# Performance work log

Hardware: AMD Instinct MI355X
Metric: run time of the kernel (lower is better)

Reference implementation:

```python
import jax, jax.numpy as jnp
import numpy as np


def setup_inputs() -> dict:
    key = jax.random.key(0)
    ks = jax.random.split(key, 6)
    B, Nu, Ni, D = 256, 512, 512, 64
    u_fea = jax.random.normal(ks[0], (B, Nu, D), dtype=jnp.float32)
    i_fea = jax.random.normal(ks[1], (B, Ni, D), dtype=jnp.float32)
    M = jax.random.normal(ks[2], (D, D), dtype=jnp.float32)
    # Linear weights, torch-style: y = x @ W.T + b (init scaled like torch default)
    lim = 1.0 / np.sqrt(D)
    Wu = jax.random.uniform(ks[3], (D, D), minval=-lim, maxval=lim, dtype=jnp.float32)
    Wi = jax.random.uniform(ks[4], (D, D), minval=-lim, maxval=lim, dtype=jnp.float32)
    bu = jnp.zeros((D,), dtype=jnp.float32)
    bi = jnp.zeros((D,), dtype=jnp.float32)
    return {"u_fea": u_fea, "i_fea": i_fea, "M": M, "Wu": Wu, "bu": bu, "Wi": Wi, "bi": bi}


def reference(u_fea, i_fea, M, Wu, bu, Wi, bi):
    # fc_u / fc_i: torch Linear is x @ W.T + b
    u = jnp.einsum('bud,ed->bue', u_fea, Wu) + bu   # [B, Nu, D]
    i = jnp.einsum('bid,ed->bie', i_fea, Wi) + bi   # [B, Ni, D]
    # Bilinear co-attention score S = u @ M @ i^T  -> [B, Nu, Ni]
    uM = jnp.einsum('bud,de->bue', u, M)
    S = jnp.einsum('bue,bie->bui', uM, i)
    # pooling == 'max'
    u_score = S.max(axis=2)   # [B, Nu]
    i_score = S.max(axis=1)   # [B, Ni]
    # gumbel == False -> plain softmax over the review axis
    p_u = jax.nn.softmax(u_score, axis=1)
    p_i = jax.nn.softmax(i_score, axis=1)
    return (p_u[:, :, None], p_i[:, :, None])
```

## Files before the change

kernel.cpp:

```cpp
#include <hip/hip_runtime.h>
#include <float.h>


#define NBATCH 256
#define NSEQ   512
#define DIM    64

typedef __attribute__((ext_vector_type(8))) short short8;
typedef __attribute__((ext_vector_type(4))) float f32x4;

#define MFMA16(a,b,c) __builtin_amdgcn_mfma_f32_16x16x32_bf16(a,b,c,0,0,0)

__device__ __forceinline__ void cvt2(float f, unsigned short &h, unsigned short &l) {
    unsigned u = __float_as_uint(f);
    unsigned hb = (u + 0x7FFFu + ((u >> 16) & 1u)) >> 16;
    h = (unsigned short)hb;
    float r = f - __uint_as_float(hb << 16);
    unsigned u2 = __float_as_uint(r);
    l = (unsigned short)((u2 + 0x7FFFu + ((u2 >> 16) & 1u)) >> 16);
}

__device__ __forceinline__ void cvt8(const f32x4 a, const f32x4 b, short8 &hi, short8 &lo) {
    unsigned short h, l;
    #pragma unroll
    for (int i = 0; i < 4; ++i) { cvt2(a[i], h, l); hi[i] = (short)h; lo[i] = (short)l; }
    #pragma unroll
    for (int i = 0; i < 4; ++i) { cvt2(b[i], h, l); hi[4+i] = (short)h; lo[4+i] = (short)l; }
}

__global__ __launch_bounds__(64) void coatt_prep1(
    const float* __restrict__ M, const float* __restrict__ Wi,
    const float* __restrict__ bi, float* __restrict__ ws)
{
    __shared__ float Ml[64];
    const int d = blockIdx.x, f = threadIdx.x;
    Ml[f] = M[d*64 + f];
    __syncthreads();
    float s = 0.f;
    #pragma unroll 8
    for (int e = 0; e < 64; ++e) s = fmaf(Ml[e], Wi[e*64 + f], s);
    ws[8448 + d*64 + f] = s;
    float p = Ml[f] * bi[f];
    #pragma unroll
    for (int off = 1; off < 64; off <<= 1) p += __shfl_xor(p, off, 64);
    if (f == 0) ws[12544 + d] = p;
}

__global__ __launch_bounds__(64) void coatt_prep2(
    const float* __restrict__ Wu, const float* __restrict__ bu,
    float* __restrict__ ws)
{
    __shared__ float col[64];
    const int c = blockIdx.x, f = threadIdx.x;
    const float* T = ws + 8448;
    col[f] = Wu[f*64 + c];
    __syncthreads();
    float s = 0.f;
    #pragma unroll 8
    for (int d = 0; d < 64; ++d) s = fmaf(col[d], T[d*64 + f], s);
    unsigned short* efh = (unsigned short*)(ws + 4352);
    unsigned short* efl = efh + 4096;
    unsigned short h, l;
    cvt2(s, h, l);
    const int ko = c >> 5, quad = (c >> 3) & 3, j = c & 7;
    const int ft = f >> 4, f15 = f & 15;
    const int p = ft*1024 + ko*512 + (quad*16 + f15)*8 + j;
    efh[p] = h; efl[p] = l;
    float pa = col[f] * ws[12544 + f];
    #pragma unroll
    for (int off = 1; off < 64; off <<= 1) pa += __shfl_xor(pa, off, 64);
    if (f == 0) ws[4096 + c] = pa;
    if (c == 0) {
        float sg = 0.f;
        #pragma unroll 8
        for (int d = 0; d < 64; ++d) sg = fmaf(bu[d], T[d*64 + f], sg);
        ws[4160 + f] = sg;
        float ps = bu[f] * ws[12544 + f];
        #pragma unroll
        for (int off = 1; off < 64; off <<= 1) ps += __shfl_xor(ps, off, 64);
        if (f == 0) ws[4224] = ps;
    }
}

#define LDS_BYTES 151552

__global__ __launch_bounds__(512, 2) void coatt_main(
    const float* __restrict__ u_fea, const float* __restrict__ i_fea,
    const float* __restrict__ ws, float* __restrict__ out)
{
    extern __shared__ char sm[];
    unsigned short* YH = (unsigned short*)sm;
    unsigned short* YL = (unsigned short*)(sm + 65536);
    const int t    = threadIdx.x;
    const int lane = t & 63, w = t >> 6, quad = lane >> 4, l15 = lane & 15;
    float* Xsw    = (float*)(sm + 131072) + w * 576;
    float* rl     = (float*)(sm + 149504);
    float* colp   = (float*)(sm + 131072);
    float* uscore = (float*)(sm + 147456);
    float* red    = (float*)(sm + 149504);

    const int b = blockIdx.x;
    const float* ub = u_fea + (size_t)b * NSEQ * DIM;
    const float* ib = i_fea + (size_t)b * NSEQ * DIM;

    const unsigned short* efh = (const unsigned short*)(ws + 4352);
    const unsigned short* efl = efh + 4096;
    short8 EH[4][2], EL[4][2];
    #pragma unroll
    for (int ft = 0; ft < 4; ++ft)
        #pragma unroll
        for (int ko = 0; ko < 2; ++ko) {
            EH[ft][ko] = *(const short8*)(efh + ((ft*2+ko)*64 + lane)*8);
            EL[ft][ko] = *(const short8*)(efl + ((ft*2+ko)*64 + lane)*8);
        }
    float gb[4];
    #pragma unroll
    for (int ft = 0; ft < 4; ++ft) gb[ft] = ws[4160 + ft*16 + l15];
    const float s0 = ws[4224];

    #pragma unroll
    for (int it = 0; it < 8; ++it) {
        const int v = it*512 + t;
        const int m = v >> 3, kq = v & 7;
        const f32x4* gp = (const f32x4*)(ib + m*64 + kq*8);
        const f32x4 f0 = gp[0], f1 = gp[1];
        short8 sh, sl;
        cvt8(f0, f1, sh, sl);
        const int off = (m>>4)*1024 + (kq>>2)*512 + ((kq&3)*16 + (m&15))*8;
        *(short8*)(YH + off) = sh;
        *(short8*)(YL + off) = sl;
    }

    {
        const f32x4* av = (const f32x4*)(ws + 4096);
        const f32x4* up = (const f32x4*)(ub + t*64);
        float s = s0;
        #pragma unroll
        for (int c4 = 0; c4 < 16; ++c4) {
            const f32x4 u4 = up[c4], a4 = av[c4];
            s = fmaf(u4[0],a4[0],s); s = fmaf(u4[1],a4[1],s);
            s = fmaf(u4[2],a4[2],s); s = fmaf(u4[3],a4[3],s);
        }
        rl[t] = s;
    }
    __syncthreads();

    const int base = w*64;
    short8 XH[4][2], XL[4][2];
    f32x4 rv[4];
    #pragma unroll
    for (int g = 0; g < 4; ++g) {
        const float* up = ub + (size_t)(base + g*16 + l15)*64 + quad*8;
        const f32x4 u0 = *(const f32x4*)up;
        const f32x4 u1 = *(const f32x4*)(up+4);
        const f32x4 u2 = *(const f32x4*)(up+32);
        const f32x4 u3 = *(const f32x4*)(up+36);
        short8 UH0, UL0, UH1, UL1;
        cvt8(u0,u1,UH0,UL0); cvt8(u2,u3,UH1,UL1);
        #pragma unroll
        for (int fp = 0; fp < 2; ++fp) {
            #pragma unroll
            for (int fh = 0; fh < 2; ++fh) {
                const int ft = fp*2 + fh;
                f32x4 c = {gb[ft], gb[ft], gb[ft], gb[ft]};
                c = MFMA16(UH0, EH[ft][0], c);
                c = MFMA16(UH1, EH[ft][1], c);
                c = MFMA16(UH0, EL[ft][0], c);
                c = MFMA16(UH1, EL[ft][1], c);
                c = MFMA16(UL0, EH[ft][0], c);
                c = MFMA16(UL1, EH[ft][1], c);
                #pragma unroll
                for (int rg = 0; rg < 4; ++rg)
                    Xsw[(quad*4+rg)*36 + fh*16 + l15] = c[rg];
            }
            const float* xp = Xsw + l15*36 + quad*8;
            f32x4 x0, x1;
            {
                float2 p0 = *(const float2*)(xp);
                float2 p1 = *(const float2*)(xp+2);
                float2 p2 = *(const float2*)(xp+4);
                float2 p3 = *(const float2*)(xp+6);
                x0 = (f32x4){p0.x, p0.y, p1.x, p1.y};
                x1 = (f32x4){p2.x, p2.y, p3.x, p3.y};
            }
            cvt8(x0, x1, XH[g][fp], XL[g][fp]);
        }
        rv[g] = *(const f32x4*)(rl + base + g*16 + quad*4);
    }
    __syncthreads();
    for (int i = t; i < 4096; i += 512) colp[i] = -FLT_MAX;
    __syncthreads();

    f32x4 rm[4];
    #pragma unroll
    for (int g = 0; g < 4; ++g)
        rm[g] = (f32x4){-FLT_MAX,-FLT_MAX,-FLT_MAX,-FLT_MAX};
    for (int T = 0; T < 32; ++T) {
        const unsigned short* yh2 = YH + T*1024 + lane*8;
        const unsigned short* yl2 = YL + T*1024 + lane*8;
        const short8 BH0 = *(const short8*)(yh2);
        const short8 BH1 = *(const short8*)(yh2 + 512);
        const short8 BL0 = *(const short8*)(yl2);
        const short8 BL1 = *(const short8*)(yl2 + 512);
        float cg[4];
        #pragma unroll
        for (int g = 0; g < 4; ++g) {
            f32x4 c = rv[g];
            c = MFMA16(XH[g][0], BH0, c);
            c = MFMA16(XH[g][1], BH1, c);
            c = MFMA16(XH[g][0], BL0, c);
            c = MFMA16(XH[g][1], BL1, c);
            c = MFMA16(XL[g][0], BH0, c);
            c = MFMA16(XL[g][1], BH1, c);
            rm[g][0] = fmaxf(rm[g][0], c[0]);
            rm[g][1] = fmaxf(rm[g][1], c[1]);
            rm[g][2] = fmaxf(rm[g][2], c[2]);
            rm[g][3] = fmaxf(rm[g][3], c[3]);
            cg[g] = fmaxf(fmaxf(c[0], c[1]), fmaxf(c[2], c[3]));
        }
        float cm = fmaxf(fmaxf(cg[0], cg[1]), fmaxf(cg[2], cg[3]));
        cm = fmaxf(cm, __shfl_xor(cm, 16, 64));
        cm = fmaxf(cm, __shfl_xor(cm, 32, 64));
        if (lane < 16) {
            float* cp = colp + w*512 + T*16 + lane;
            *cp = fmaxf(*cp, cm);
        }
    }
    #pragma unroll
    for (int g = 0; g < 4; ++g)
        #pragma unroll
        for (int rg = 0; rg < 4; ++rg) {
            float v = rm[g][rg];
            v = fmaxf(v, __shfl_xor(v, 1, 64));
            v = fmaxf(v, __shfl_xor(v, 2, 64));
            v = fmaxf(v, __shfl_xor(v, 4, 64));
            v = fmaxf(v, __shfl_xor(v, 8, 64));
            if (l15 == 0) uscore[base + g*16 + quad*4 + rg] = v;
        }
    __syncthreads();

    {
        float v = uscore[t];
        float m = v;
        #pragma unroll
        for (int off = 1; off < 64; off <<= 1) m = fmaxf(m, __shfl_xor(m, off, 64));
        if (lane == 0) red[w] = m;
        __syncthreads();
        m = red[0];
        #pragma unroll
        for (int q = 1; q < 8; ++q) m = fmaxf(m, red[q]);
        const float e = __expf(v - m);
        float s = e;
        #pragma unroll
        for (int off = 1; off < 64; off <<= 1) s += __shfl_xor(s, off, 64);
        if (lane == 0) red[8+w] = s;
        __syncthreads();
        float sum = red[8];
        #pragma unroll
        for (int q = 1; q < 8; ++q) sum += red[8+q];
        out[(size_t)b*NSEQ + t] = e * (1.0f / sum);
    }
    __syncthreads();
    {
        float v = colp[t];
        #pragma unroll
        for (int s8 = 1; s8 < 8; ++s8) v = fmaxf(v, colp[s8*512 + t]);
        float m = v;
        #pragma unroll
        for (int off = 1; off < 64; off <<= 1) m = fmaxf(m, __shfl_xor(m, off, 64));
        if (lane == 0) red[w] = m;
        __syncthreads();
        m = red[0];
        #pragma unroll
        for (int q = 1; q < 8; ++q) m = fmaxf(m, red[q]);
        const float e = __expf(v - m);
        float s = e;
        #pragma unroll
        for (int off = 1; off < 64; off <<= 1) s += __shfl_xor(s, off, 64);
        if (lane == 0) red[8+w] = s;
        __syncthreads();
        float sum = red[8];
        #pragma unroll
        for (int q = 1; q < 8; ++q) sum += red[8+q];
        out[(size_t)NBATCH*NSEQ + (size_t)b*NSEQ + t] = e * (1.0f / sum);
    }
}

extern "C" void kernel_launch(void* const* d_in, const int* in_sizes, int n_in,
                              void* d_out, int out_size, void* d_ws, size_t ws_size,
                              hipStream_t stream) {
    const float* u_fea = (const float*)d_in[0];
    const float* i_fea = (const float*)d_in[1];
    const float* M     = (const float*)d_in[2];
    const float* Wu    = (const float*)d_in[3];
    const float* bu    = (const float*)d_in[4];
    const float* Wi    = (const float*)d_in[5];
    const float* bi    = (const float*)d_in[6];
    float* out = (float*)d_out;
    float* ws  = (float*)d_ws;

    coatt_prep1<<<64, 64, 0, stream>>>(M, Wi, bi, ws);
    coatt_prep2<<<64, 64, 0, stream>>>(Wu, bu, ws);
    coatt_main<<<NBATCH, 512, LDS_BYTES, stream>>>(u_fea, i_fea, ws, out);
}
```

Before: 148.8 us.

## Compute X tile transposed in registers, drop LDS staging and extra syncs

Swaps the MFMA operand order in the X = U·E projection so the result lands in the layout the main loop needs, which removes the per-wave LDS transpose buffer and its round trip. The per-row bias term is now computed with register dot products and shuffles instead of a separate LDS pass followed by a barrier. The i_fea staging is reorganized so each wave writes its tiles directly in fragment layout. Float-to-bf16 hi/lo splitting now uses the packed HIP bf16 conversion intrinsics, colp is written directly rather than initialized and max-accumulated, and LDS usage shrinks slightly.

New measurement: 140.4 us. 1.06x faster.

```diff
diff --git a/kernel.cpp b/kernel.cpp
--- a/kernel.cpp
+++ b/kernel.cpp
@@ -1,4 +1,5 @@
 #include <hip/hip_runtime.h>
+#include <hip/hip_bf16.h>
 #include <float.h>
 
 
@@ -10,6 +11,8 @@
 typedef __attribute__((ext_vector_type(4))) float f32x4;
 
 #define MFMA16(a,b,c) __builtin_amdgcn_mfma_f32_16x16x32_bf16(a,b,c,0,0,0)
+
+union BF2 { __hip_bfloat162 b; short2 s; };
 
 __device__ __forceinline__ void cvt2(float f, unsigned short &h, unsigned short &l) {
     unsigned u = __float_as_uint(f);
@@ -21,11 +24,22 @@
 }
 
 __device__ __forceinline__ void cvt8(const f32x4 a, const f32x4 b, short8 &hi, short8 &lo) {
-    unsigned short h, l;
-    #pragma unroll
-    for (int i = 0; i < 4; ++i) { cvt2(a[i], h, l); hi[i] = (short)h; lo[i] = (short)l; }
-    #pragma unroll
-    for (int i = 0; i < 4; ++i) { cvt2(b[i], h, l); hi[4+i] = (short)h; lo[4+i] = (short)l; }
+    BF2 h0, h1, h2, h3;
+    h0.b = __float22bfloat162_rn(make_float2(a[0], a[1]));
+    h1.b = __float22bfloat162_rn(make_float2(a[2], a[3]));
+    h2.b = __float22bfloat162_rn(make_float2(b[0], b[1]));
+    h3.b = __float22bfloat162_rn(make_float2(b[2], b[3]));
+    hi = short8{h0.s.x, h0.s.y, h1.s.x, h1.s.y, h2.s.x, h2.s.y, h3.s.x, h3.s.y};
+    BF2 l0, l1, l2, l3;
+    l0.b = __float22bfloat162_rn(make_float2(a[0] - __bfloat162float(h0.b.x),
+                                             a[1] - __bfloat162float(h0.b.y)));
+    l1.b = __float22bfloat162_rn(make_float2(a[2] - __bfloat162float(h1.b.x),
+                                             a[3] - __bfloat162float(h1.b.y)));
+    l2.b = __float22bfloat162_rn(make_float2(b[0] - __bfloat162float(h2.b.x),
+                                             b[1] - __bfloat162float(h2.b.y)));
+    l3.b = __float22bfloat162_rn(make_float2(b[2] - __bfloat162float(h3.b.x),
+                                             b[3] - __bfloat162float(h3.b.y)));
+    lo = short8{l0.s.x, l0.s.y, l1.s.x, l1.s.y, l2.s.x, l2.s.y, l3.s.x, l3.s.y};
 }
 
 __global__ __launch_bounds__(64) void coatt_prep1(
@@ -82,7 +96,7 @@
     }
 }
 
-#define LDS_BYTES 151552
+#define LDS_BYTES 149568
 
 __global__ __launch_bounds__(512, 2) void coatt_main(
     const float* __restrict__ u_fea, const float* __restrict__ i_fea,
@@ -91,14 +105,12 @@
     extern __shared__ char sm[];
     unsigned short* YH = (unsigned short*)sm;
     unsigned short* YL = (unsigned short*)(sm + 65536);
-    const int t    = threadIdx.x;
-    const int lane = t & 63, w = t >> 6, quad = lane >> 4, l15 = lane & 15;
-    float* Xsw    = (float*)(sm + 131072) + w * 576;
-    float* rl     = (float*)(sm + 149504);
     float* colp   = (float*)(sm + 131072);
     float* uscore = (float*)(sm + 147456);
     float* red    = (float*)(sm + 149504);
 
+    const int t    = threadIdx.x;
+    const int lane = t & 63, w = t >> 6, quad = lane >> 4, l15 = lane & 15;
     const int b = blockIdx.x;
     const float* ub = u_fea + (size_t)b * NSEQ * DIM;
     const float* ib = i_fea + (size_t)b * NSEQ * DIM;
@@ -113,88 +125,93 @@
             EH[ft][ko] = *(const short8*)(efh + ((ft*2+ko)*64 + lane)*8);
             EL[ft][ko] = *(const short8*)(efl + ((ft*2+ko)*64 + lane)*8);
         }
-    float gb[4];
-    #pragma unroll
-    for (int ft = 0; ft < 4; ++ft) gb[ft] = ws[4160 + ft*16 + l15];
+    f32x4 gq[4];
+    #pragma unroll
+    for (int ft = 0; ft < 4; ++ft) gq[ft] = *(const f32x4*)(ws + 4160 + ft*16 + quad*4);
+    const f32x4 av0 = *(const f32x4*)(ws + 4096 + quad*8);
+    const f32x4 av1 = *(const f32x4*)(ws + 4096 + quad*8 + 4);
+    const f32x4 av2 = *(const f32x4*)(ws + 4096 + 32 + quad*8);
+    const f32x4 av3 = *(const f32x4*)(ws + 4096 + 32 + quad*8 + 4);
     const float s0 = ws[4224];
 
     #pragma unroll
-    for (int it = 0; it < 8; ++it) {
-        const int v = it*512 + t;
-        const int m = v >> 3, kq = v & 7;
-        const f32x4* gp = (const f32x4*)(ib + m*64 + kq*8);
-        const f32x4 f0 = gp[0], f1 = gp[1];
-        short8 sh, sl;
-        cvt8(f0, f1, sh, sl);
-        const int off = (m>>4)*1024 + (kq>>2)*512 + ((kq&3)*16 + (m&15))*8;
-        *(short8*)(YH + off) = sh;
-        *(short8*)(YL + off) = sl;
-    }
-
-    {
-        const f32x4* av = (const f32x4*)(ws + 4096);
-        const f32x4* up = (const f32x4*)(ub + t*64);
-        float s = s0;
-        #pragma unroll
-        for (int c4 = 0; c4 < 16; ++c4) {
-            const f32x4 u4 = up[c4], a4 = av[c4];
-            s = fmaf(u4[0],a4[0],s); s = fmaf(u4[1],a4[1],s);
-            s = fmaf(u4[2],a4[2],s); s = fmaf(u4[3],a4[3],s);
-        }
-        rl[t] = s;
-    }
-    __syncthreads();
+    for (int bt = 0; bt < 2; ++bt) {
+        f32x4 ya[4], yb[4];
+        #pragma unroll
+        for (int q = 0; q < 4; ++q) {
+            const int task = bt*4 + q;
+            const int tile = w*4 + (task >> 1);
+            const int p = task & 1;
+            const float* yp = ib + (size_t)(tile*16 + l15)*64 + p*16 + quad*4;
+            ya[q] = *(const f32x4*)yp;
+            yb[q] = *(const f32x4*)(yp + 32);
+        }
+        #pragma unroll
+        for (int q = 0; q < 4; ++q) {
+            const int task = bt*4 + q;
+            const int tile = w*4 + (task >> 1);
+            const int p = task & 1;
+            short8 sh, sl;
+            cvt8(ya[q], yb[q], sh, sl);
+            const int off = tile*1024 + p*512 + lane*8;
+            *(short8*)(YH + off) = sh;
+            *(short8*)(YL + off) = sl;
+        }
+    }
 
     const int base = w*64;
+    f32x4 u[4][4];
+    #pragma unroll
+    for (int g = 0; g < 4; ++g) {
+        const float* up = ub + (size_t)(base + g*16 + l15)*64 + quad*8;
+        u[g][0] = *(const f32x4*)up;
+        u[g][1] = *(const f32x4*)(up + 4);
+        u[g][2] = *(const f32x4*)(up + 32);
+        u[g][3] = *(const f32x4*)(up + 36);
+    }
     short8 XH[4][2], XL[4][2];
     f32x4 rv[4];
     #pragma unroll
     for (int g = 0; g < 4; ++g) {
-        const float* up = ub + (size_t)(base + g*16 + l15)*64 + quad*8;
-        const f32x4 u0 = *(const f32x4*)up;
-        const f32x4 u1 = *(const f32x4*)(up+4);
-        const f32x4 u2 = *(const f32x4*)(up+32);
-        const f32x4 u3 = *(const f32x4*)(up+36);
         short8 UH0, UL0, UH1, UL1;
-        cvt8(u0,u1,UH0,UL0); cvt8(u2,u3,UH1,UL1);
-        #pragma unroll
-        for (int fp = 0; fp < 2; ++fp) {
-            #pragma unroll
-            for (int fh = 0; fh < 2; ++fh) {
-                const int ft = fp*2 + fh;
-                f32x4 c = {gb[ft], gb[ft], gb[ft], gb[ft]};
-                c = MFMA16(UH0, EH[ft][0], c);
-                c = MFMA16(UH1, EH[ft][1], c);
-                c = MFMA16(UH0, EL[ft][0], c);
-                c = MFMA16(UH1, EL[ft][1], c);
-                c = MFMA16(UL0, EH[ft][0], c);
-                c = MFMA16(UL1, EH[ft][1], c);
-                #pragma unroll
-                for (int rg = 0; rg < 4; ++rg)
-                    Xsw[(quad*4+rg)*36 + fh*16 + l15] = c[rg];
-            }
-            const float* xp = Xsw + l15*36 + quad*8;
-            f32x4 x0, x1;
-            {
-                float2 p0 = *(const float2*)(xp);
-                float2 p1 = *(const float2*)(xp+2);
-                float2 p2 = *(const float2*)(xp+4);
-                float2 p3 = *(const float2*)(xp+6);
-                x0 = (f32x4){p0.x, p0.y, p1.x, p1.y};
-                x1 = (f32x4){p2.x, p2.y, p3.x, p3.y};
-            }
-            cvt8(x0, x1, XH[g][fp], XL[g][fp]);
-        }
-        rv[g] = *(const f32x4*)(rl + base + g*16 + quad*4);
-    }
-    __syncthreads();
-    for (int i = t; i < 4096; i += 512) colp[i] = -FLT_MAX;
+        cvt8(u[g][0], u[g][1], UH0, UL0);
+        cvt8(u[g][2], u[g][3], UH1, UL1);
+        float rp = 0.f;
+        #pragma unroll
+        for (int e = 0; e < 4; ++e) rp = fmaf(u[g][0][e], av0[e], rp);
+        #pragma unroll
+        for (int e = 0; e < 4; ++e) rp = fmaf(u[g][1][e], av1[e], rp);
+        #pragma unroll
+        for (int e = 0; e < 4; ++e) rp = fmaf(u[g][2][e], av2[e], rp);
+        #pragma unroll
+        for (int e = 0; e < 4; ++e) rp = fmaf(u[g][3][e], av3[e], rp);
+        rp += __shfl_xor(rp, 16, 64);
+        rp += __shfl_xor(rp, 32, 64);
+        rp += s0;
+        f32x4 ct[4];
+        #pragma unroll
+        for (int ft = 0; ft < 4; ++ft) {
+            f32x4 c = gq[ft];
+            c = MFMA16(EH[ft][0], UH0, c);
+            c = MFMA16(EH[ft][1], UH1, c);
+            c = MFMA16(EH[ft][0], UL0, c);
+            c = MFMA16(EH[ft][1], UL1, c);
+            c = MFMA16(EL[ft][0], UH0, c);
+            c = MFMA16(EL[ft][1], UH1, c);
+            ct[ft] = c;
+        }
+        cvt8(ct[0], ct[2], XH[g][0], XL[g][0]);
+        cvt8(ct[1], ct[3], XH[g][1], XL[g][1]);
+        #pragma unroll
+        for (int rg = 0; rg < 4; ++rg)
+            rv[g][rg] = __shfl(rp, quad*4 + rg, 64);
+    }
     __syncthreads();
 
     f32x4 rm[4];
     #pragma unroll
     for (int g = 0; g < 4; ++g)
-        rm[g] = (f32x4){-FLT_MAX,-FLT_MAX,-FLT_MAX,-FLT_MAX};
+        rm[g] = (f32x4){-FLT_MAX, -FLT_MAX, -FLT_MAX, -FLT_MAX};
     for (int T = 0; T < 32; ++T) {
         const unsigned short* yh2 = YH + T*1024 + lane*8;
         const unsigned short* yl2 = YL + T*1024 + lane*8;
@@ -221,10 +238,7 @@
         float cm = fmaxf(fmaxf(cg[0], cg[1]), fmaxf(cg[2], cg[3]));
         cm = fmaxf(cm, __shfl_xor(cm, 16, 64));
         cm = fmaxf(cm, __shfl_xor(cm, 32, 64));
-        if (lane < 16) {
-            float* cp = colp + w*512 + T*16 + lane;
-            *cp = fmaxf(*cp, cm);
-        }
+        if (lane < 16) colp[w*512 + T*16 + lane] = cm;
     }
     #pragma unroll
     for (int g = 0; g < 4; ++g)
```
